# Performance work log

Hardware: AMD Instinct MI355X
Metric: run time of the kernel (lower is better)

## Reference

```python
import jax, jax.numpy as jnp
import numpy as np

N_NODES = 50000
N_EDGES = 800000
IN_FEATS = 256
NUM_HEADS = 8
OUT_FEATS = 32
NEG_SLOPE = 0.2


def setup_inputs() -> dict:
    key = jax.random.key(0)
    ks = jax.random.split(key, 10)
    feat = jax.random.normal(ks[0], (N_NODES, IN_FEATS), dtype=jnp.float32)
    edge_emb = jax.random.normal(ks[1], (N_EDGES, NUM_HEADS), dtype=jnp.float32)
    src = jax.random.randint(ks[2], (N_EDGES,), 0, N_NODES, dtype=jnp.int32)
    dst = jax.random.randint(ks[3], (N_EDGES,), 0, N_NODES, dtype=jnp.int32)
    # learned params (xavier-style scale)
    W_src = jax.random.normal(ks[4], (IN_FEATS, NUM_HEADS * OUT_FEATS), dtype=jnp.float32) * 0.05
    W_e = jax.random.normal(ks[5], (NUM_HEADS, NUM_HEADS * OUT_FEATS), dtype=jnp.float32) * 0.3
    attn_l = jax.random.normal(ks[6], (NUM_HEADS, OUT_FEATS), dtype=jnp.float32) * 0.2
    attn_r = jax.random.normal(ks[7], (NUM_HEADS, OUT_FEATS), dtype=jnp.float32) * 0.2
    attn_e = jax.random.normal(ks[8], (NUM_HEADS, OUT_FEATS), dtype=jnp.float32) * 0.2
    bias = jnp.zeros((NUM_HEADS * OUT_FEATS,), dtype=jnp.float32)
    return {"feat": feat, "edge_emb": edge_emb, "src": src, "dst": dst,
            "W_src": W_src, "W_e": W_e, "attn_l": attn_l, "attn_r": attn_r,
            "attn_e": attn_e, "bias": bias}


def reference(feat, edge_emb, src, dst, W_src, W_e, attn_l, attn_r, attn_e, bias):
    N = feat.shape[0]
    H, D = attn_l.shape
    # node projections (share_weights=True -> fc_dst is fc_src)
    h = (feat @ W_src).reshape(N, H, D)            # (N, H, D)
    ef = (edge_emb @ W_e).reshape(-1, H, D)        # (E, H, D)
    # per-head attention scalars
    el = jnp.einsum("nhd,hd->nh", h, attn_l)      # (N, H)
    er = jnp.einsum("nhd,hd->nh", h, attn_r)      # (N, H)
    ee = jnp.einsum("ehd,hd->eh", ef, attn_e)     # (E, H)
    logits = jax.nn.leaky_relu(el[src] + er[dst] + ee, NEG_SLOPE)  # (E, H)
    # edge softmax over incoming edges of each dst node (numerically stable)
    m = jax.ops.segment_max(logits, dst, num_segments=N)
    m = jnp.where(jnp.isfinite(m), m, 0.0)
    p = jnp.exp(logits - m[dst])
    s = jax.ops.segment_sum(p, dst, num_segments=N)
    alpha = p / (s[dst] + 1e-9)                    # (E, H)
    # weighted message aggregation
    out = jax.ops.segment_sum(alpha[:, :, None] * h[src], dst, num_segments=N)  # (N, H, D)
    out = out + bias.reshape(1, H, D)
    return out
```

## Files before the change

kernel.cpp:

```cpp
#include <hip/hip_runtime.h>

#define H 8
#define D 32
#define HD 256
#define NEG_SLOPE 0.2f
#define SCB 1024

typedef __attribute__((ext_vector_type(8))) short bf8;
typedef __attribute__((ext_vector_type(4))) float f4;

__device__ __forceinline__ unsigned short f2b(float x) {
    unsigned u = __float_as_uint(x);
    unsigned r = (u + 0x7fffu + ((u >> 16) & 1u)) >> 16;
    return (unsigned short)r;
}

__global__ __launch_bounds__(256) void k0(
        const float* __restrict__ W, unsigned short* __restrict__ Wtb,
        const float* __restrict__ W_e, const float* __restrict__ attn_e,
        float* __restrict__ M, int* __restrict__ cnt, int N) {
    const int b = blockIdx.x, t = threadIdx.x;
    if (b < HD) {
        Wtb[b * HD + t] = f2b(W[t * HD + b]);
    } else if (b == HD) {
        if (t < 64) {
            int k = t >> 3, hh = t & 7;
            float acc = 0.f;
            for (int d = 0; d < D; ++d)
                acc = fmaf(W_e[k * HD + hh * D + d], attn_e[hh * D + d], acc);
            M[k * 8 + hh] = acc;
        }
    } else {
        int i = (b - HD - 1) * 256 + t;
        if (i < N) cnt[i] = 0;
    }
}

__global__ __launch_bounds__(1024) void k_scan1(const int* __restrict__ cnt,
                                                int* __restrict__ offs,
                                                int* __restrict__ btot, int N) {
    __shared__ int wtot[16], wbase[16];
    const int t = threadIdx.x, wid = t >> 6, lane = t & 63;
    int i = blockIdx.x * SCB + t;
    int v = (i < N) ? cnt[i] : 0;
    int x = v;
#pragma unroll
    for (int off = 1; off < 64; off <<= 1) {
        int y = __shfl_up(x, off, 64);
        if (lane >= off) x += y;
    }
    if (lane == 63) wtot[wid] = x;
    __syncthreads();
    if (t < 16) {
        int w = wtot[t], xs = w;
#pragma unroll
        for (int off = 1; off < 16; off <<= 1) {
            int y = __shfl_up(xs, off, 64);
            if (t >= off) xs += y;
        }
        wbase[t] = xs - w;
        if (t == 15) btot[blockIdx.x] = xs;
    }
    __syncthreads();
    if (i < N) offs[i] = wbase[wid] + (x - v);
}

__global__ __launch_bounds__(1024) void k_scan3(int* __restrict__ offs,
                                                const int* __restrict__ btot,
                                                int* __restrict__ cur,
                                                int N, int E, int nb) {
    __shared__ int bb;
    const int t = threadIdx.x;
    if (t < 64) {
        int vv = (t < nb) ? btot[t] : 0;
        int x = vv;
#pragma unroll
        for (int off = 1; off < 64; off <<= 1) {
            int y = __shfl_up(x, off, 64);
            if (t >= off) x += y;
        }
        if (t == blockIdx.x) bb = x - vv;
    }
    __syncthreads();
    const int i = blockIdx.x * SCB + t;
    if (i < N) {
        const int o = offs[i] + bb;
        offs[i] = o;
        cur[i] = o;
    }
    if (i == 0) offs[N] = E;
}

__global__ __launch_bounds__(512) void k_fuse(
        const float* __restrict__ feat, const unsigned short* __restrict__ Wtb,
        const float* __restrict__ attn_l, const float* __restrict__ attn_r,
        unsigned short* __restrict__ hb, float* __restrict__ el,
        float* __restrict__ er, int N, int bg,
        const int* __restrict__ dst, int* __restrict__ cnt, int E) {
    const int t = threadIdx.x;
    if (blockIdx.x >= bg) {
        const int base = (blockIdx.x - bg) * 2048;
        const int end = min(base + 2048, E);
        for (int e = base + t; e < end; e += 512)
            atomicAdd(&cnt[dst[e]], 1);
        return;
    }
    __shared__ unsigned short lwt[128 * HD];
    const int l = t & 63, wv = t >> 6;
    const int row0 = (blockIdx.x * 8 + wv) * 16;
    const bool act = row0 < N;
    const int m = l & 15, q = l >> 4;

    bf8 afr[8];
    if (act) {
        const float* arow = feat + (size_t)(row0 + m) * HD + q * 8;
#pragma unroll
        for (int kc = 0; kc < 8; ++kc) {
            const float4 f0 = *(const float4*)(arow + kc * 32);
            const float4 f1 = *(const float4*)(arow + kc * 32 + 4);
            bf8 a;
            a[0] = (short)f2b(f0.x); a[1] = (short)f2b(f0.y);
            a[2] = (short)f2b(f0.z); a[3] = (short)f2b(f0.w);
            a[4] = (short)f2b(f1.x); a[5] = (short)f2b(f1.y);
            a[6] = (short)f2b(f1.z); a[7] = (short)f2b(f1.w);
            afr[kc] = a;
        }
    }

    f4 acc[16];
#pragma unroll
    for (int nt = 0; nt < 16; ++nt) acc[nt] = (f4){0.f, 0.f, 0.f, 0.f};

    const uint4* wt4 = (const uint4*)Wtb;
    uint4* l4 = (uint4*)lwt;
#pragma unroll
    for (int half = 0; half < 2; ++half) {
        if (half) __syncthreads();
#pragma unroll
        for (int i = 0; i < 8; ++i) {
            const int u = i * 512 + t;
            l4[u ^ ((u >> 5) & 7)] = wt4[half * 4096 + u];
        }
        __syncthreads();
        if (act) {
#pragma unroll
            for (int ntl = 0; ntl < 8; ++ntl) {
                const int nt = half * 8 + ntl;
                const int lc = ntl * 16 + m;
                const unsigned short* bp = lwt + lc * HD;
                const int sw = (lc & 7) * 8;
#pragma unroll
                for (int kc = 0; kc < 8; ++kc) {
                    const bf8 b = *(const bf8*)(bp + ((q * 8 + kc * 32) ^ sw));
                    acc[nt] = __builtin_amdgcn_mfma_f32_16x16x32_bf16(
                                  afr[kc], b, acc[nt], 0, 0, 0);
                }
            }
        }
    }
    if (!act) return;

#pragma unroll
    for (int h = 0; h < H; ++h) {
        float elp[4] = {0.f, 0.f, 0.f, 0.f};
        float erp[4] = {0.f, 0.f, 0.f, 0.f};
#pragma unroll
        for (int s = 0; s < 2; ++s) {
            const int nt = h * 2 + s;
            const int c = nt * 16 + m;
            const float alc = attn_l[c];
            const float arc = attn_r[c];
#pragma unroll
            for (int reg = 0; reg < 4; ++reg) {
                const float v = acc[nt][reg];
                hb[(size_t)(row0 + q * 4 + reg) * HD + c] = f2b(v);
                elp[reg] = fmaf(v, alc, elp[reg]);
                erp[reg] = fmaf(v, arc, erp[reg]);
            }
        }
#pragma unroll
        for (int reg = 0; reg < 4; ++reg) {
#pragma unroll
            for (int off = 1; off < 16; off <<= 1) {
                elp[reg] += __shfl_xor(elp[reg], off, 16);
                erp[reg] += __shfl_xor(erp[reg], off, 16);
            }
        }
        if (m == 0) {
#pragma unroll
            for (int reg = 0; reg < 4; ++reg) {
                el[(row0 + q * 4 + reg) * H + h] = elp[reg];
                er[(row0 + q * 4 + reg) * H + h] = erp[reg];
            }
        }
    }
}

__global__ __launch_bounds__(256) void k_edge(
        const int* __restrict__ src, const int* __restrict__ dst,
        const float* __restrict__ edge_emb, const float* __restrict__ el,
        const float* __restrict__ Mg, int* __restrict__ cur,
        int* __restrict__ src_csr, float* __restrict__ lgcsr, int E) {
    const int t = threadIdx.x;
    float Mreg[8][8];
#pragma unroll
    for (int k = 0; k < 8; ++k) {
        const float4 m0 = *(const float4*)(Mg + k * 8);
        const float4 m1 = *(const float4*)(Mg + k * 8 + 4);
        Mreg[k][0] = m0.x; Mreg[k][1] = m0.y; Mreg[k][2] = m0.z; Mreg[k][3] = m0.w;
        Mreg[k][4] = m1.x; Mreg[k][5] = m1.y; Mreg[k][6] = m1.z; Mreg[k][7] = m1.w;
    }
    const int base = blockIdx.x * 1024;
    const int end = min(base + 1024, E);
    for (int e = base + t; e < end; e += 256) {
        const int se = src[e], de = dst[e];
        const float4 e0 = ((const float4*)edge_emb)[e * 2];
        const float4 e1 = ((const float4*)edge_emb)[e * 2 + 1];
        const float4 l0 = ((const float4*)el)[se * 2];
        const float4 l1 = ((const float4*)el)[se * 2 + 1];
        const float ee[8] = {e0.x, e0.y, e0.z, e0.w, e1.x, e1.y, e1.z, e1.w};
        const float ela[8] = {l0.x, l0.y, l0.z, l0.w, l1.x, l1.y, l1.z, l1.w};
        float lg[8];
#pragma unroll
        for (int hh = 0; hh < 8; ++hh) {
            float x = ela[hh];
#pragma unroll
            for (int k = 0; k < 8; ++k)
                x = fmaf(ee[k], Mreg[k][hh], x);
            lg[hh] = x;
        }
        const int p = atomicAdd(&cur[de], 1);
        src_csr[p] = se;
        float4* o = (float4*)&lgcsr[(size_t)p * 8];
        o[0] = make_float4(lg[0], lg[1], lg[2], lg[3]);
        o[1] = make_float4(lg[4], lg[5], lg[6], lg[7]);
    }
}

__global__ __launch_bounds__(256) void k_node(
        const int* __restrict__ offs, const int* __restrict__ src_csr,
        const float* __restrict__ lgcsr, const float* __restrict__ er,
        const unsigned short* __restrict__ hb, const float* __restrict__ bias,
        float* __restrict__ out, int N) {
    const int t = threadIdx.x;
    const int lane = t & 63;
    const int v = blockIdx.x * 4 + (t >> 6);
    if (v >= N) return;
    const int hh = lane & 7;
    const int sl = lane & 31;
    const int half = lane >> 5;
    const int cb = sl * 8;
    const int hq = sl >> 2;
    const int s0 = offs[v];
    const int deg = offs[v + 1] - s0;

    const float erv = er[(size_t)v * 8 + hh];
    const unsigned short* hbc = hb + cb;

    float a[8];
#pragma unroll
    for (int i = 0; i < 8; ++i) a[i] = 0.f;
    float psum = 0.f;

    for (int j0 = 0; j0 < deg; j0 += 64) {
        const int nj = min(64, deg - j0);
        int srcl = 0;
        if (lane < nj) srcl = src_csr[s0 + j0 + lane];
        const float* lgb = lgcsr + (size_t)(s0 + j0) * 8;

        float pv[8];
#pragma unroll
        for (int s = 0; s < 8; ++s) {
            pv[s] = 0.f;
            if (s * 8 < nj) {
                const int j = s * 8 + (lane >> 3);
                if (j < nj) {
                    float x = lgb[s * 64 + lane] + erv;
                    x = (x >= 0.f) ? x : NEG_SLOPE * x;
                    pv[s] = __expf(x);
                    psum += pv[s];
                }
            }
        }

#pragma unroll
        for (int g = 0; g < 4; ++g) {
            if (g * 16 >= nj) break;
            int sx8[8];
            uint4 w8[8];
#pragma unroll
            for (int i = 0; i < 8; ++i) {
                const int s = 2 * g + (i >> 2);
                const int jj = 2 * (i & 3) + half;
                sx8[i] = __shfl(srcl, s * 8 + jj, 64);
                w8[i] = *(const uint4*)(hbc + (size_t)sx8[i] * HD);
            }
#pragma unroll
            for (int i = 0; i < 8; ++i) {
                const int s = 2 * g + (i >> 2);
                const int jj = 2 * (i & 3) + half;
                const float pj = __shfl(pv[s], jj * 8 + hq, 64);
                const uint4 w = w8[i];
                a[0] = fmaf(pj, __uint_as_float(w.x << 16), a[0]);
                a[1] = fmaf(pj, __uint_as_float(w.x & 0xffff0000u), a[1]);
                a[2] = fmaf(pj, __uint_as_float(w.y << 16), a[2]);
                a[3] = fmaf(pj, __uint_as_float(w.y & 0xffff0000u), a[3]);
                a[4] = fmaf(pj, __uint_as_float(w.z << 16), a[4]);
                a[5] = fmaf(pj, __uint_as_float(w.z & 0xffff0000u), a[5]);
                a[6] = fmaf(pj, __uint_as_float(w.w << 16), a[6]);
                a[7] = fmaf(pj, __uint_as_float(w.w & 0xffff0000u), a[7]);
            }
        }
    }

#pragma unroll
    for (int i = 0; i < 8; ++i) a[i] += __shfl_xor(a[i], 32, 64);

    psum += __shfl_xor(psum, 8, 64);
    psum += __shfl_xor(psum, 16, 64);
    psum += __shfl_xor(psum, 32, 64);
    const float rs = 1.f / (__shfl(psum, hq, 8) + 1e-9f);
    if (half == 0) {
        const float4 b0 = *(const float4*)&bias[cb];
        const float4 b1 = *(const float4*)&bias[cb + 4];
        *(float4*)&out[(size_t)v * HD + cb] =
            make_float4(fmaf(a[0], rs, b0.x), fmaf(a[1], rs, b0.y),
                        fmaf(a[2], rs, b0.z), fmaf(a[3], rs, b0.w));
        *(float4*)&out[(size_t)v * HD + cb + 4] =
            make_float4(fmaf(a[4], rs, b1.x), fmaf(a[5], rs, b1.y),
                        fmaf(a[6], rs, b1.z), fmaf(a[7], rs, b1.w));
    }
}

extern "C" void kernel_launch(void* const* d_in, const int* in_sizes, int n_in,
                              void* d_out, int out_size, void* d_ws, size_t ws_size,
                              hipStream_t stream) {
    const float* feat     = (const float*)d_in[0];
    const float* edge_emb = (const float*)d_in[1];
    const int*   src      = (const int*)d_in[2];
    const int*   dst      = (const int*)d_in[3];
    const float* W_src    = (const float*)d_in[4];
    const float* W_e      = (const float*)d_in[5];
    const float* attn_l   = (const float*)d_in[6];
    const float* attn_r   = (const float*)d_in[7];
    const float* attn_e   = (const float*)d_in[8];
    const float* bias     = (const float*)d_in[9];
    float* out = (float*)d_out;

    const int N = in_sizes[0] / HD;
    const int E = in_sizes[2];

    char* ws = (char*)d_ws;
    unsigned short* hb = (unsigned short*)ws; ws += (size_t)N * HD * 2;
    float* lgcsr = (float*)ws; ws += (size_t)E * H * 4;
    int* src_csr = (int*)ws; ws += (size_t)E * 4;
    float* el   = (float*)ws; ws += (size_t)N * H * 4;
    float* er   = (float*)ws; ws += (size_t)N * H * 4;
    int*   cnt  = (int*)ws;   ws += (size_t)N * 4;
    int*   cur  = cnt;
    int* offs   = (int*)ws; ws += (size_t)(N + 1) * 4;
    unsigned short* Wtb = (unsigned short*)ws; ws += (size_t)HD * HD * 2;
    int* btot  = (int*)ws; ws += 64 * 4;
    float* M   = (float*)ws; ws += 256;

    const int nz  = (N + 255) / 256;
    const int nsb = (N + SCB - 1) / SCB;
    const int bg  = ((N + 15) / 16 + 7) / 8;
    const int bhist = (E + 2047) / 2048;

    k0      <<<HD + 1 + nz, 256, 0, stream>>>(W_src, Wtb, W_e, attn_e, M, cnt, N);
    k_fuse  <<<bg + bhist, 512, 0, stream>>>(feat, Wtb, attn_l, attn_r, hb, el, er,
                                             N, bg, dst, cnt, E);
    k_scan1 <<<nsb, SCB, 0, stream>>>(cnt, offs, btot, N);
    k_scan3 <<<nsb, SCB, 0, stream>>>(offs, btot, cur, N, E, nsb);
    k_edge  <<<(E + 1023) / 1024, 256, 0, stream>>>(src, dst, edge_emb, el, M,
                                                    cur, src_csr, lgcsr, E);
    k_node  <<<(N + 3) / 4, 256, 0, stream>>>(offs, src_csr, lgcsr, er,
                                              hb, bias, out, N);
}
```

Baseline: 301.6 us.

## Record per-edge slot during histogram to drop second atomic pass in CSR build

The histogram atomicAdd now stores its return value as each edge's rank within its destination bucket. The edge kernel computes its CSR position as offs[dst] + ord[e] instead of issuing a second contended atomicAdd on a cursor array. The edge kernel also moves to one edge per thread and reads the 8x8 matrix straight from global memory rather than preloading it into registers. This costs an extra E-sized int array written and read, but removes a round of global atomics and the cursor copy in the scan.

```diff
diff --git a/kernel.cpp b/kernel.cpp
--- a/kernel.cpp
+++ b/kernel.cpp
@@ -67,7 +67,6 @@
 
 __global__ __launch_bounds__(1024) void k_scan3(int* __restrict__ offs,
                                                 const int* __restrict__ btot,
-                                                int* __restrict__ cur,
                                                 int N, int E, int nb) {
     __shared__ int bb;
     const int t = threadIdx.x;
@@ -83,11 +82,7 @@
     }
     __syncthreads();
     const int i = blockIdx.x * SCB + t;
-    if (i < N) {
-        const int o = offs[i] + bb;
-        offs[i] = o;
-        cur[i] = o;
-    }
+    if (i < N) offs[i] += bb;
     if (i == 0) offs[N] = E;
 }
 
@@ -96,13 +91,14 @@
         const float* __restrict__ attn_l, const float* __restrict__ attn_r,
         unsigned short* __restrict__ hb, float* __restrict__ el,
         float* __restrict__ er, int N, int bg,
-        const int* __restrict__ dst, int* __restrict__ cnt, int E) {
+        const int* __restrict__ dst, int* __restrict__ cnt,
+        int* __restrict__ ord, int E) {
     const int t = threadIdx.x;
     if (blockIdx.x >= bg) {
         const int base = (blockIdx.x - bg) * 2048;
         const int end = min(base + 2048, E);
         for (int e = base + t; e < end; e += 512)
-            atomicAdd(&cnt[dst[e]], 1);
+            ord[e] = atomicAdd(&cnt[dst[e]], 1);
         return;
     }
     __shared__ unsigned short lwt[128 * HD];
@@ -199,42 +195,32 @@
 __global__ __launch_bounds__(256) void k_edge(
         const int* __restrict__ src, const int* __restrict__ dst,
         const float* __restrict__ edge_emb, const float* __restrict__ el,
-        const float* __restrict__ Mg, int* __restrict__ cur,
+        const float* __restrict__ Mg, const int* __restrict__ offs,
+        const int* __restrict__ ord,
         int* __restrict__ src_csr, float* __restrict__ lgcsr, int E) {
-    const int t = threadIdx.x;
-    float Mreg[8][8];
-#pragma unroll
-    for (int k = 0; k < 8; ++k) {
-        const float4 m0 = *(const float4*)(Mg + k * 8);
-        const float4 m1 = *(const float4*)(Mg + k * 8 + 4);
-        Mreg[k][0] = m0.x; Mreg[k][1] = m0.y; Mreg[k][2] = m0.z; Mreg[k][3] = m0.w;
-        Mreg[k][4] = m1.x; Mreg[k][5] = m1.y; Mreg[k][6] = m1.z; Mreg[k][7] = m1.w;
-    }
-    const int base = blockIdx.x * 1024;
-    const int end = min(base + 1024, E);
-    for (int e = base + t; e < end; e += 256) {
-        const int se = src[e], de = dst[e];
-        const float4 e0 = ((const float4*)edge_emb)[e * 2];
-        const float4 e1 = ((const float4*)edge_emb)[e * 2 + 1];
-        const float4 l0 = ((const float4*)el)[se * 2];
-        const float4 l1 = ((const float4*)el)[se * 2 + 1];
-        const float ee[8] = {e0.x, e0.y, e0.z, e0.w, e1.x, e1.y, e1.z, e1.w};
-        const float ela[8] = {l0.x, l0.y, l0.z, l0.w, l1.x, l1.y, l1.z, l1.w};
-        float lg[8];
-#pragma unroll
-        for (int hh = 0; hh < 8; ++hh) {
-            float x = ela[hh];
-#pragma unroll
-            for (int k = 0; k < 8; ++k)
-                x = fmaf(ee[k], Mreg[k][hh], x);
-            lg[hh] = x;
-        }
-        const int p = atomicAdd(&cur[de], 1);
-        src_csr[p] = se;
-        float4* o = (float4*)&lgcsr[(size_t)p * 8];
-        o[0] = make_float4(lg[0], lg[1], lg[2], lg[3]);
-        o[1] = make_float4(lg[4], lg[5], lg[6], lg[7]);
-    }
+    const int e = blockIdx.x * 256 + threadIdx.x;
+    if (e >= E) return;
+    const int se = src[e], de = dst[e];
+    const float4 e0 = ((const float4*)edge_emb)[e * 2];
+    const float4 e1 = ((const float4*)edge_emb)[e * 2 + 1];
+    const float4 l0 = ((const float4*)el)[se * 2];
+    const float4 l1 = ((const float4*)el)[se * 2 + 1];
+    const float ee[8] = {e0.x, e0.y, e0.z, e0.w, e1.x, e1.y, e1.z, e1.w};
+    const float ela[8] = {l0.x, l0.y, l0.z, l0.w, l1.x, l1.y, l1.z, l1.w};
+    float lg[8];
+#pragma unroll
+    for (int hh = 0; hh < 8; ++hh) {
+        float x = ela[hh];
+#pragma unroll
+        for (int k = 0; k < 8; ++k)
+            x = fmaf(ee[k], Mg[k * 8 + hh], x);
+        lg[hh] = x;
+    }
+    const int p = offs[de] + ord[e];
+    src_csr[p] = se;
+    float4* o = (float4*)&lgcsr[(size_t)p * 8];
+    o[0] = make_float4(lg[0], lg[1], lg[2], lg[3]);
+    o[1] = make_float4(lg[4], lg[5], lg[6], lg[7]);
 }
 
 __global__ __launch_bounds__(256) void k_node(
@@ -354,10 +340,10 @@
     unsigned short* hb = (unsigned short*)ws; ws += (size_t)N * HD * 2;
     float* lgcsr = (float*)ws; ws += (size_t)E * H * 4;
     int* src_csr = (int*)ws; ws += (size_t)E * 4;
+    int* ord     = (int*)ws; ws += (size_t)E * 4;
     float* el   = (float*)ws; ws += (size_t)N * H * 4;
     float* er   = (float*)ws; ws += (size_t)N * H * 4;
     int*   cnt  = (int*)ws;   ws += (size_t)N * 4;
-    int*   cur  = cnt;
     int* offs   = (int*)ws; ws += (size_t)(N + 1) * 4;
     unsigned short* Wtb = (unsigned short*)ws; ws += (size_t)HD * HD * 2;
     int* btot  = (int*)ws; ws += 64 * 4;
@@ -370,11 +356,11 @@
 
     k0      <<<HD + 1 + nz, 256, 0, stream>>>(W_src, Wtb, W_e, attn_e, M, cnt, N);
     k_fuse  <<<bg + bhist, 512, 0, stream>>>(feat, Wtb, attn_l, attn_r, hb, el, er,
-                                             N, bg, dst, cnt, E);
+                                             N, bg, dst, cnt, ord, E);
     k_scan1 <<<nsb, SCB, 0, stream>>>(cnt, offs, btot, N);
-    k_scan3 <<<nsb, SCB, 0, stream>>>(offs, btot, cur, N, E, nsb);
-    k_edge  <<<(E + 1023) / 1024, 256, 0, stream>>>(src, dst, edge_emb, el, M,
-                                                    cur, src_csr, lgcsr, E);
+    k_scan3 <<<nsb, SCB, 0, stream>>>(offs, btot, N, E, nsb);
+    k_edge  <<<(E + 255) / 256, 256, 0, stream>>>(src, dst, edge_emb, el, M,
+                                                  offs, ord, src_csr, lgcsr, E);
     k_node  <<<(N + 3) / 4, 256, 0, stream>>>(offs, src_csr, lgcsr, er,
                                               hb, bias, out, N);
 }
```

Result: faster. 282.2 us (-6.4%).
